# Kernel tuning notes

Hardware: AMD Instinct MI355X
Metric: run time of the kernel (lower is better)

The kernel has to match this reference:

```python
import jax, jax.numpy as jnp
import numpy as np

D_MODEL = 1024
HEADS = 16
D_K = D_MODEL // HEADS
D_FF = 4096
B, S = 2, 2048
EPS = 1e-5


def setup_inputs() -> dict:
    key = jax.random.key(0)
    ks = jax.random.split(key, 16)
    sc_att = 1.0 / np.sqrt(D_MODEL)
    sc_ff1 = 1.0 / np.sqrt(D_MODEL)
    sc_ff2 = 1.0 / np.sqrt(D_FF)
    return {
        "input": jax.random.normal(ks[0], (B, S, D_MODEL), jnp.float32),
        "mask": jnp.ones((B, 1, 1, S), jnp.int32),
        # stacked per-head projections: [H, D_MODEL, D_K]
        "Wq": jax.random.normal(ks[1], (HEADS, D_MODEL, D_K), jnp.float32) * sc_att,
        "bq": jax.random.normal(ks[2], (HEADS, D_K), jnp.float32) * 0.01,
        "Wk": jax.random.normal(ks[3], (HEADS, D_MODEL, D_K), jnp.float32) * sc_att,
        "bk": jax.random.normal(ks[4], (HEADS, D_K), jnp.float32) * 0.01,
        "Wv": jax.random.normal(ks[5], (HEADS, D_MODEL, D_K), jnp.float32) * sc_att,
        "bv": jax.random.normal(ks[6], (HEADS, D_K), jnp.float32) * 0.01,
        "Wo": jax.random.normal(ks[7], (D_MODEL, D_MODEL), jnp.float32) * sc_att,
        "bo": jax.random.normal(ks[8], (D_MODEL,), jnp.float32) * 0.01,
        "ln1_g": jnp.ones((D_MODEL,), jnp.float32),
        "ln1_b": jnp.zeros((D_MODEL,), jnp.float32),
        "ln2_g": jnp.ones((D_MODEL,), jnp.float32),
        "ln2_b": jnp.zeros((D_MODEL,), jnp.float32),
        "W1": jax.random.normal(ks[9], (D_MODEL, D_FF), jnp.float32) * sc_ff1,
        "b1": jax.random.normal(ks[10], (D_FF,), jnp.float32) * 0.01,
        "W2": jax.random.normal(ks[11], (D_FF, D_MODEL), jnp.float32) * sc_ff2,
        "b2": jax.random.normal(ks[12], (D_MODEL,), jnp.float32) * 0.01,
    }


def _layernorm(x, g, b):
    mu = jnp.mean(x, axis=-1, keepdims=True)
    var = jnp.mean(jnp.square(x - mu), axis=-1, keepdims=True)
    return (x - mu) * jax.lax.rsqrt(var + EPS) * g + b


def reference(input, mask, Wq, bq, Wk, bk, Wv, bv, Wo, bo,
              ln1_g, ln1_b, ln2_g, ln2_b, W1, b1, W2, b2):
    x = input
    # per-head projections, stacked: [B,H,S,D_K]
    q = jnp.einsum('bsd,hdk->bhsk', x, Wq) + bq[None, :, None, :]
    k = jnp.einsum('bsd,hdk->bhsk', x, Wk) + bk[None, :, None, :]
    v = jnp.einsum('bsd,hdk->bhsk', x, Wv) + bv[None, :, None, :]
    scores = jnp.einsum('bhqk,bhsk->bhqs', q, k) / np.sqrt(D_K)  # [B,H,S,S]
    scores = jnp.where(mask == 0, jnp.float32(-1e9), scores)
    attn = jax.nn.softmax(scores, axis=-1)
    ctx = jnp.einsum('bhqs,bhsk->bhqk', attn, v)  # [B,H,S,D_K]
    # concat heads along feature dim (head h occupies slice h*D_K:(h+1)*D_K)
    ctx = jnp.transpose(ctx, (0, 2, 1, 3)).reshape(B, S, D_MODEL)
    att_out = ctx @ Wo + bo
    h = _layernorm(x + att_out, ln1_g, ln1_b)
    ff = jax.nn.relu(h @ W1 + b1) @ W2 + b2
    return _layernorm(h + ff, ln2_g, ln2_b)
```

## Files before the change

kernel.cpp:

```cpp
#include <hip/hip_runtime.h>
#include <cstdint>
#include <cstddef>

typedef unsigned short u16;
typedef unsigned int   u32;
typedef unsigned short u16x4 __attribute__((ext_vector_type(4)));
typedef unsigned short u16x8 __attribute__((ext_vector_type(8)));
typedef unsigned int   u32x2 __attribute__((ext_vector_type(2)));
typedef __bf16 bf16x8 __attribute__((ext_vector_type(8)));
typedef float f32x4 __attribute__((ext_vector_type(4)));

#define MFMA16(a, b, c) __builtin_amdgcn_mfma_f32_16x16x32_bf16((a), (b), (c), 0, 0, 0)

__device__ __forceinline__ float bf2f(u16 h) {
  union { unsigned u; float f; } v; v.u = ((unsigned)h) << 16; return v.f;
}
__device__ __forceinline__ u16 f2bf(float f) {
  union { float f; unsigned u; } v; v.f = f;
  unsigned r = v.u + 0x7fffu + ((v.u >> 16) & 1u);
  return (u16)(r >> 16);
}
__device__ __forceinline__ void gll16(const u16* g, u16* l) {
  __builtin_amdgcn_global_load_lds(
      (const __attribute__((address_space(1))) void*)g,
      (__attribute__((address_space(3))) void*)l, 16, 0, 0);
}
__device__ __forceinline__ float fast_exp2(float x) {
#if __has_builtin(__builtin_amdgcn_exp2f)
  return __builtin_amdgcn_exp2f(x);
#else
  return exp2f(x);
#endif
}

__global__ __launch_bounds__(256) void transpose_qkv(
    const float* __restrict__ Wq, const float* __restrict__ Wk,
    const float* __restrict__ Wv, u16* __restrict__ outb) {
  __shared__ u16 tile[32][33];
  const int z = blockIdx.z;
  const int which = z >> 4, h = z & 15;
  const float* in = (which == 0 ? Wq : (which == 1 ? Wk : Wv)) + (size_t)h * 1024 * 64;
  u16* out = outb + ((size_t)which * 1024 + h * 64) * 1024;
  const int tx = threadIdx.x & 31, ty = threadIdx.x >> 5;
  const int r0 = blockIdx.y * 32, c0 = blockIdx.x * 32;
  #pragma unroll
  for (int i = 0; i < 32; i += 8)
    tile[ty + i][tx] = f2bf(in[(size_t)(r0 + ty + i) * 64 + c0 + tx]);
  __syncthreads();
  #pragma unroll
  for (int i = 0; i < 32; i += 8)
    out[(size_t)(c0 + ty + i) * 1024 + r0 + tx] = tile[tx][ty + i];
}

__global__ __launch_bounds__(256) void transpose_w(
    const float* __restrict__ Wo, const float* __restrict__ W1,
    const float* __restrict__ W2, u16* __restrict__ Wo_t,
    u16* __restrict__ W1_t, u16* __restrict__ W2_t) {
  __shared__ u16 tile[32][33];
  const int id = blockIdx.x;
  const float* in; u16* outp; int R, C, cx, ry;
  if (id < 1024)      { in = Wo; outp = Wo_t; R = 1024; C = 1024; cx = id & 31;  ry = id >> 5; }
  else if (id < 5120) { int t = id - 1024; in = W1; outp = W1_t; R = 1024; C = 4096; cx = t & 127; ry = t >> 7; }
  else                { int t = id - 5120; in = W2; outp = W2_t; R = 4096; C = 1024; cx = t & 31;  ry = t >> 5; }
  const int tx = threadIdx.x & 31, ty = threadIdx.x >> 5;
  const int r0 = ry * 32, c0 = cx * 32;
  #pragma unroll
  for (int i = 0; i < 32; i += 8)
    tile[ty + i][tx] = f2bf(in[(size_t)(r0 + ty + i) * C + c0 + tx]);
  __syncthreads();
  #pragma unroll
  for (int i = 0; i < 32; i += 8)
    outp[(size_t)(c0 + ty + i) * R + r0 + tx] = tile[tx][ty + i];
}

__global__ __launch_bounds__(256) void prep_small(
    const float* __restrict__ bq, const float* __restrict__ bk,
    const float* __restrict__ bv, const int* __restrict__ mask,
    float* __restrict__ biasq, float* __restrict__ madd2) {
  int i = blockIdx.x * 256 + threadIdx.x;
  if (i < 3072) {
    biasq[i] = (i < 1024) ? bq[i] : (i < 2048 ? bk[i - 1024] : bv[i - 2048]);
  } else if (i < 7168) {
    int j = i - 3072;
    madd2[j] = mask[j] ? -23.083120f : -1.442695e9f;
  }
}

__global__ __launch_bounds__(256) void cvt_x(
    const float* __restrict__ in, u16* __restrict__ out, int n) {
  int i = (blockIdx.x * 256 + threadIdx.x) * 4;
  if (i >= n) return;
  const float4 v = *(const float4*)&in[i];
  u16x4 o;
  o[0] = f2bf(v.x); o[1] = f2bf(v.y); o[2] = f2bf(v.z); o[3] = f2bf(v.w);
  *(u16x4*)&out[i] = o;
}

template <int MODE>
__global__ __launch_bounds__(256) void gemm_bt(
    const u16* __restrict__ A, const u16* __restrict__ Bt,
    const float* __restrict__ bias, u16* __restrict__ C,
    int M, int N, int K) {
  __shared__ __align__(16) u16 As[2][128 * 32];
  __shared__ __align__(16) u16 Bs[2][128 * 32];
  const int tid = threadIdx.x;
  const int lane = tid & 63;
  const int wave = tid >> 6;
  const int m0 = blockIdx.y * 128;
  const int n0 = blockIdx.x * 128;
  const int wr = (wave >> 1) * 64;
  const int wc = (wave & 1) * 64;
  const int lrow = lane & 15;
  const int quad = lane >> 4;

  const int srow = lane >> 2;
  const int scol = (lane & 3) * 8;
  const u16* gA1 = &A[(size_t)(m0 + wave * 16 + srow) * K + scol];
  const u16* gA2 = &A[(size_t)(m0 + 64 + wave * 16 + srow) * K + scol];
  const u16* gB1 = &Bt[(size_t)(n0 + wave * 16 + srow) * K + scol];
  const u16* gB2 = &Bt[(size_t)(n0 + 64 + wave * 16 + srow) * K + scol];
  const int so1 = (wave * 16) * 32;
  const int so2 = (wave * 16 + 64) * 32;

  f32x4 acc[4][4];
  #pragma unroll
  for (int i = 0; i < 4; ++i)
    #pragma unroll
    for (int j = 0; j < 4; ++j)
      acc[i][j] = (f32x4){0.f, 0.f, 0.f, 0.f};

  for (int k0 = 0; k0 < K; k0 += 64) {
    gll16(gA1 + k0, &As[0][so1]);
    gll16(gA2 + k0, &As[0][so2]);
    gll16(gB1 + k0, &Bs[0][so1]);
    gll16(gB2 + k0, &Bs[0][so2]);
    gll16(gA1 + k0 + 32, &As[1][so1]);
    gll16(gA2 + k0 + 32, &As[1][so2]);
    gll16(gB1 + k0 + 32, &Bs[1][so1]);
    gll16(gB2 + k0 + 32, &Bs[1][so2]);
    __syncthreads();
    #pragma unroll
    for (int kb = 0; kb < 2; ++kb) {
      bf16x8 af[4], bfr[4];
      #pragma unroll
      for (int i = 0; i < 4; ++i) {
        af[i]  = *(const bf16x8*)&As[kb][(wr + i * 16 + lrow) * 32 + quad * 8];
        bfr[i] = *(const bf16x8*)&Bs[kb][(wc + i * 16 + lrow) * 32 + quad * 8];
      }
      #pragma unroll
      for (int fr = 0; fr < 4; ++fr)
        #pragma unroll
        for (int fc = 0; fc < 4; ++fc)
          acc[fr][fc] = MFMA16(af[fr], bfr[fc], acc[fr][fc]);
    }
    __syncthreads();
  }

  #pragma unroll
  for (int fr = 0; fr < 4; ++fr) {
    int rowb = m0 + wr + fr * 16 + quad * 4;
    #pragma unroll
    for (int fc = 0; fc < 4; ++fc) {
      int col = n0 + wc + fc * 16 + lrow;
      float bv = bias[col];
      #pragma unroll
      for (int r = 0; r < 4; ++r) {
        float v = acc[fr][fc][r] + bv;
        if (MODE == 1) v = fmaxf(v, 0.f);
        C[(size_t)(rowb + r) * N + col] = f2bf(v);
      }
    }
  }
}

__global__ __launch_bounds__(256) void gemm_splitk(
    const u16* __restrict__ A, const u16* __restrict__ Bt,
    u16* __restrict__ Cp, int M, int N, int K) {
  __shared__ __align__(16) u16 As[2][128 * 32];
  __shared__ __align__(16) u16 Bs[2][128 * 32];
  const int tid = threadIdx.x;
  const int lane = tid & 63;
  const int wave = tid >> 6;
  const int m0 = blockIdx.y * 128;
  const int n0 = blockIdx.x * 128;
  const int kz = blockIdx.z;
  const int Kh = K >> 1;
  const int kbase = kz * Kh;
  const int wr = (wave >> 1) * 64;
  const int wc = (wave & 1) * 64;
  const int lrow = lane & 15;
  const int quad = lane >> 4;

  const int srow = lane >> 2;
  const int scol = (lane & 3) * 8;
  const u16* gA1 = &A[(size_t)(m0 + wave * 16 + srow) * K + kbase + scol];
  const u16* gA2 = &A[(size_t)(m0 + 64 + wave * 16 + srow) * K + kbase + scol];
  const u16* gB1 = &Bt[(size_t)(n0 + wave * 16 + srow) * K + kbase + scol];
  const u16* gB2 = &Bt[(size_t)(n0 + 64 + wave * 16 + srow) * K + kbase + scol];
  const int so1 = (wave * 16) * 32;
  const int so2 = (wave * 16 + 64) * 32;
  u16* C = Cp + (size_t)kz * M * N;

  f32x4 acc[4][4];
  #pragma unroll
  for (int i = 0; i < 4; ++i)
    #pragma unroll
    for (int j = 0; j < 4; ++j)
      acc[i][j] = (f32x4){0.f, 0.f, 0.f, 0.f};

  for (int k0 = 0; k0 < Kh; k0 += 64) {
    gll16(gA1 + k0, &As[0][so1]);
    gll16(gA2 + k0, &As[0][so2]);
    gll16(gB1 + k0, &Bs[0][so1]);
    gll16(gB2 + k0, &Bs[0][so2]);
    gll16(gA1 + k0 + 32, &As[1][so1]);
    gll16(gA2 + k0 + 32, &As[1][so2]);
    gll16(gB1 + k0 + 32, &Bs[1][so1]);
    gll16(gB2 + k0 + 32, &Bs[1][so2]);
    __syncthreads();
    #pragma unroll
    for (int kb = 0; kb < 2; ++kb) {
      bf16x8 af[4], bfr[4];
      #pragma unroll
      for (int i = 0; i < 4; ++i) {
        af[i]  = *(const bf16x8*)&As[kb][(wr + i * 16 + lrow) * 32 + quad * 8];
        bfr[i] = *(const bf16x8*)&Bs[kb][(wc + i * 16 + lrow) * 32 + quad * 8];
      }
      #pragma unroll
      for (int fr = 0; fr < 4; ++fr)
        #pragma unroll
        for (int fc = 0; fc < 4; ++fc)
          acc[fr][fc] = MFMA16(af[fr], bfr[fc], acc[fr][fc]);
    }
    __syncthreads();
  }

  #pragma unroll
  for (int fr = 0; fr < 4; ++fr) {
    int rowb = m0 + wr + fr * 16 + quad * 4;
    #pragma unroll
    for (int fc = 0; fc < 4; ++fc) {
      int col = n0 + wc + fc * 16 + lrow;
      #pragma unroll
      for (int r = 0; r < 4; ++r)
        C[(size_t)(rowb + r) * N + col] = f2bf(acc[fr][fc][r]);
    }
  }
}

__global__ __launch_bounds__(256) void attn_kernel(
    const u16* __restrict__ xqkv, const float* __restrict__ madd2,
    u16* __restrict__ ctx) {
  __shared__ __align__(16) u16 Ks[64][72];
  __shared__ __align__(16) u16 Vt[64][136];
  __shared__ __align__(16) u16 Ps[4][2][16][72];
  const int tid = threadIdx.x;
  const int lane = tid & 63;
  const int wave = tid >> 6;
  const int lrow = lane & 15;
  const int quad = lane >> 4;
  const int b = blockIdx.z, h = blockIdx.y;
  const int qb = blockIdx.x * 128 + wave * 16;
  const u16* Qp = xqkv + (size_t)b * 2048 * 3072 + h * 64;
  const u16* Kp = Qp + 1024;
  const u16* Vp = Qp + 2048;
  const float S2 = 0.18033688f;

  bf16x8 qa[2][2];
  #pragma unroll
  for (int t = 0; t < 2; ++t) {
    qa[t][0] = *(const bf16x8*)&Qp[(size_t)(qb + t * 64 + lrow) * 3072 + quad * 8];
    qa[t][1] = *(const bf16x8*)&Qp[(size_t)(qb + t * 64 + lrow) * 3072 + 32 + quad * 8];
  }

  f32x4 o[2][4];
  #pragma unroll
  for (int t = 0; t < 2; ++t)
    #pragma unroll
    for (int i = 0; i < 4; ++i) o[t][i] = (f32x4){0.f, 0.f, 0.f, 0.f};
  float rsum[2] = {0.f, 0.f};

  const int ks_row = tid >> 3, ks_col = (tid & 7) * 8;
  const int v_dg = tid >> 4;
  const int v_kp = tid & 15;
  const float* maddb = madd2 + b * 2048;

  u16x8 kreg[2];
  u16x4 va[2], vb[2];
  #pragma unroll
  for (int sh = 0; sh < 2; ++sh) {
    kreg[sh] = *(const u16x8*)&Kp[(size_t)(sh * 32 + ks_row) * 3072 + ks_col];
    va[sh] = *(const u16x4*)&Vp[(size_t)(sh * 32 + 2 * v_kp) * 3072 + v_dg * 4];
    vb[sh] = *(const u16x4*)&Vp[(size_t)(sh * 32 + 2 * v_kp + 1) * 3072 + v_dg * 4];
  }

  for (int s0 = 0; s0 < 2048; s0 += 64) {
    __syncthreads();
    #pragma unroll
    for (int sh = 0; sh < 2; ++sh) {
      *(u16x8*)&Ks[sh * 32 + ks_row][ks_col] = kreg[sh];
      #pragma unroll
      for (int j = 0; j < 4; ++j) {
        u32 pk = ((u32)vb[sh][j] << 16) | (u32)va[sh][j];
        *(u32*)&Vt[v_dg * 4 + j][sh * 32 + 2 * v_kp] = pk;
      }
    }
    __syncthreads();
    if (s0 + 64 < 2048) {
      #pragma unroll
      for (int sh = 0; sh < 2; ++sh) {
        int sb = s0 + 64 + sh * 32;
        kreg[sh] = *(const u16x8*)&Kp[(size_t)(sb + ks_row) * 3072 + ks_col];
        va[sh] = *(const u16x4*)&Vp[(size_t)(sb + 2 * v_kp) * 3072 + v_dg * 4];
        vb[sh] = *(const u16x4*)&Vp[(size_t)(sb + 2 * v_kp + 1) * 3072 + v_dg * 4];
      }
    }

    bf16x8 kf[4][2], vf[4][2];
    #pragma unroll
    for (int kb = 0; kb < 4; ++kb) {
      kf[kb][0] = *(const bf16x8*)&Ks[kb * 16 + lrow][quad * 8];
      kf[kb][1] = *(const bf16x8*)&Ks[kb * 16 + lrow][32 + quad * 8];
    }
    #pragma unroll
    for (int nb = 0; nb < 4; ++nb) {
      vf[nb][0] = *(const bf16x8*)&Vt[nb * 16 + lrow][quad * 8];
      vf[nb][1] = *(const bf16x8*)&Vt[nb * 16 + lrow][32 + quad * 8];
    }

    #pragma unroll
    for (int t = 0; t < 2; ++t) {
      #pragma unroll
      for (int kb = 0; kb < 4; ++kb) {
        f32x4 z = (f32x4){0.f, 0.f, 0.f, 0.f};
        z = MFMA16(kf[kb][0], qa[t][0], z);
        z = MFMA16(kf[kb][1], qa[t][1], z);
        f32x4 m4 = *(const f32x4*)&maddb[s0 + kb * 16 + quad * 4];
        u32 pb[4];
        #pragma unroll
        for (int r = 0; r < 4; ++r) {
          float p = fast_exp2(fmaf(z[r], S2, m4[r]));
          rsum[t] += p;
          union { float f; u32 u; } cv; cv.f = p;
          pb[r] = cv.u + 0x8000u;
        }
        u32x2 w2;
        w2[0] = __builtin_amdgcn_perm(pb[1], pb[0], 0x07060302);
        w2[1] = __builtin_amdgcn_perm(pb[3], pb[2], 0x07060302);
        *(u32x2*)&Ps[wave][t][lrow][kb * 16 + quad * 4] = w2;
      }
      #pragma unroll
      for (int kh = 0; kh < 2; ++kh) {
        bf16x8 pa = *(const bf16x8*)&Ps[wave][t][lrow][kh * 32 + quad * 8];
        #pragma unroll
        for (int nb = 0; nb < 4; ++nb)
          o[t][nb] = MFMA16(pa, vf[nb][kh], o[t][nb]);
      }
    }
  }

  #pragma unroll
  for (int t = 0; t < 2; ++t) {
    float rs = rsum[t];
    rs += __shfl_xor(rs, 16, 64);
    rs += __shfl_xor(rs, 32, 64);
    float inv = 1.f / fmaxf(rs, 1e-30f);
    #pragma unroll
    for (int r = 0; r < 4; ++r) {
      float invq = __shfl(inv, quad * 4 + r, 64);
      int q = qb + t * 64 + quad * 4 + r;
      #pragma unroll
      for (int nb = 0; nb < 4; ++nb) {
        float v = o[t][nb][r] * invq;
        ctx[((size_t)b * 2048 + q) * 1024 + h * 64 + nb * 16 + lrow] = f2bf(v);
      }
    }
  }
}

template <int IN_BF, int OUT_BF>
__global__ __launch_bounds__(256) void add_ln2p(
    const void* __restrict__ xa_, const u16* __restrict__ p0,
    const u16* __restrict__ p1, const float* __restrict__ cb,
    const float* __restrict__ g, const float* __restrict__ bb,
    void* __restrict__ outp_) {
  __shared__ float red[8];
  const int tid = threadIdx.x;
  const size_t base = (size_t)blockIdx.x * 1024;
  const float* xf = (const float*)xa_;
  const u16*   xb = (const u16*)xa_;
  float v[4];
  float s = 0.f;
  #pragma unroll
  for (int i = 0; i < 4; ++i) {
    int c = i * 256 + tid;
    float xv = IN_BF ? bf2f(xb[base + c]) : xf[base + c];
    v[i] = xv + bf2f(p0[base + c]) + bf2f(p1[base + c]) + cb[c];
    s += v[i];
  }
  #pragma unroll
  for (int off = 32; off > 0; off >>= 1) s += __shfl_down(s, off, 64);
  if ((tid & 63) == 0) red[tid >> 6] = s;
  __syncthreads();
  float mean = (red[0] + red[1] + red[2] + red[3]) * (1.f / 1024.f);
  float s2 = 0.f;
  #pragma unroll
  for (int i = 0; i < 4; ++i) { float d = v[i] - mean; s2 += d * d; }
  #pragma unroll
  for (int off = 32; off > 0; off >>= 1) s2 += __shfl_down(s2, off, 64);
  if ((tid & 63) == 0) red[4 + (tid >> 6)] = s2;
  __syncthreads();
  float var = (red[4] + red[5] + red[6] + red[7]) * (1.f / 1024.f);
  float rstd = rsqrtf(var + 1e-5f);
  #pragma unroll
  for (int i = 0; i < 4; ++i) {
    int c = i * 256 + tid;
    float r = (v[i] - mean) * rstd * g[c] + bb[c];
    if (OUT_BF) ((u16*)outp_)[base + c] = f2bf(r);
    else        ((float*)outp_)[base + c] = r;
  }
}

extern "C" void kernel_launch(void* const* d_in, const int* in_sizes, int n_in,
                              void* d_out, int out_size, void* d_ws, size_t ws_size,
                              hipStream_t stream) {
  (void)in_sizes; (void)n_in; (void)out_size; (void)ws_size;
  const float* x    = (const float*)d_in[0];
  const int*   mask = (const int*)d_in[1];
  const float* Wq   = (const float*)d_in[2];
  const float* bq   = (const float*)d_in[3];
  const float* Wk   = (const float*)d_in[4];
  const float* bk   = (const float*)d_in[5];
  const float* Wv   = (const float*)d_in[6];
  const float* bv   = (const float*)d_in[7];
  const float* Wo   = (const float*)d_in[8];
  const float* bo   = (const float*)d_in[9];
  const float* ln1g = (const float*)d_in[10];
  const float* ln1b = (const float*)d_in[11];
  const float* ln2g = (const float*)d_in[12];
  const float* ln2b = (const float*)d_in[13];
  const float* W1   = (const float*)d_in[14];
  const float* b1   = (const float*)d_in[15];
  const float* W2   = (const float*)d_in[16];
  const float* b2   = (const float*)d_in[17];
  float* out = (float*)d_out;

  char* ws = (char*)d_ws;
  u16*   Wqkv_t = (u16*)(ws + 0);
  u16*   fp     = (u16*)(ws + 0);
  u16*   Wo_t   = (u16*)(ws + 6291456);
  u16*   W1_t   = (u16*)(ws + 8388608);
  u16*   W2_t   = (u16*)(ws + 16777216);
  u16*   xqkv   = (u16*)(ws + 25165824);
  u16*   wp     = (u16*)(ws + 25165824);
  u16*   xb     = (u16*)(ws + 50331648);
  u16*   ctx    = (u16*)(ws + 50331648);
  u16*   ff1    = (u16*)(ws + 25165824);
  u16*   hbuf   = (u16*)(ws + 67108864);
  float* biasq  = (float*)(ws + 75497472);
  float* madd2  = (float*)(ws + 75509760);

  prep_small<<<28, 256, 0, stream>>>(bq, bk, bv, mask, biasq, madd2);
  transpose_qkv<<<dim3(2, 32, 48), 256, 0, stream>>>(Wq, Wk, Wv, Wqkv_t);
  transpose_w<<<9216, 256, 0, stream>>>(Wo, W1, W2, Wo_t, W1_t, W2_t);
  cvt_x<<<4096, 256, 0, stream>>>(x, xb, 4194304);

  gemm_bt<0><<<dim3(24, 32), 256, 0, stream>>>(xb, Wqkv_t, biasq, xqkv,
                                               4096, 3072, 1024);
  attn_kernel<<<dim3(16, 16, 2), 256, 0, stream>>>(xqkv, madd2, ctx);
  gemm_splitk<<<dim3(8, 32, 2), 256, 0, stream>>>(ctx, Wo_t, wp, 4096, 1024, 1024);
  add_ln2p<0, 1><<<4096, 256, 0, stream>>>(x, wp, wp + 4194304, bo,
                                           ln1g, ln1b, hbuf);
  gemm_bt<1><<<dim3(32, 32), 256, 0, stream>>>(hbuf, W1_t, b1, ff1,
                                               4096, 4096, 1024);
  gemm_splitk<<<dim3(8, 32, 2), 256, 0, stream>>>(ff1, W2_t, fp, 4096, 1024, 4096);
  add_ln2p<1, 0><<<4096, 256, 0, stream>>>(hbuf, fp, fp + 4194304, b2,
                                           ln2g, ln2b, out);
}
```

Before: 379.2 us.

## Fold softmax scale into Q weights, halve attention rows per block, add MFMA priority

```diff
diff --git a/kernel.cpp b/kernel.cpp
--- a/kernel.cpp
+++ b/kernel.cpp
@@ -41,11 +41,12 @@
   const int which = z >> 4, h = z & 15;
   const float* in = (which == 0 ? Wq : (which == 1 ? Wk : Wv)) + (size_t)h * 1024 * 64;
   u16* out = outb + ((size_t)which * 1024 + h * 64) * 1024;
+  const float sc = (which == 0) ? 0.18033688f : 1.0f;
   const int tx = threadIdx.x & 31, ty = threadIdx.x >> 5;
   const int r0 = blockIdx.y * 32, c0 = blockIdx.x * 32;
   #pragma unroll
   for (int i = 0; i < 32; i += 8)
-    tile[ty + i][tx] = f2bf(in[(size_t)(r0 + ty + i) * 64 + c0 + tx]);
+    tile[ty + i][tx] = f2bf(in[(size_t)(r0 + ty + i) * 64 + c0 + tx] * sc);
   __syncthreads();
   #pragma unroll
   for (int i = 0; i < 32; i += 8)
@@ -79,7 +80,8 @@
     float* __restrict__ biasq, float* __restrict__ madd2) {
   int i = blockIdx.x * 256 + threadIdx.x;
   if (i < 3072) {
-    biasq[i] = (i < 1024) ? bq[i] : (i < 2048 ? bk[i - 1024] : bv[i - 2048]);
+    biasq[i] = (i < 1024) ? bq[i] * 0.18033688f
+                          : (i < 2048 ? bk[i - 1024] : bv[i - 2048]);
   } else if (i < 7168) {
     int j = i - 3072;
     madd2[j] = mask[j] ? -23.083120f : -1.442695e9f;
@@ -253,32 +255,25 @@
     u16* __restrict__ ctx) {
   __shared__ __align__(16) u16 Ks[64][72];
   __shared__ __align__(16) u16 Vt[64][136];
-  __shared__ __align__(16) u16 Ps[4][2][16][72];
+  __shared__ __align__(16) u16 Ps[4][16][72];
   const int tid = threadIdx.x;
   const int lane = tid & 63;
   const int wave = tid >> 6;
   const int lrow = lane & 15;
   const int quad = lane >> 4;
   const int b = blockIdx.z, h = blockIdx.y;
-  const int qb = blockIdx.x * 128 + wave * 16;
+  const int qb = blockIdx.x * 64 + wave * 16;
   const u16* Qp = xqkv + (size_t)b * 2048 * 3072 + h * 64;
   const u16* Kp = Qp + 1024;
   const u16* Vp = Qp + 2048;
-  const float S2 = 0.18033688f;
-
-  bf16x8 qa[2][2];
-  #pragma unroll
-  for (int t = 0; t < 2; ++t) {
-    qa[t][0] = *(const bf16x8*)&Qp[(size_t)(qb + t * 64 + lrow) * 3072 + quad * 8];
-    qa[t][1] = *(const bf16x8*)&Qp[(size_t)(qb + t * 64 + lrow) * 3072 + 32 + quad * 8];
-  }
-
-  f32x4 o[2][4];
-  #pragma unroll
-  for (int t = 0; t < 2; ++t)
-    #pragma unroll
-    for (int i = 0; i < 4; ++i) o[t][i] = (f32x4){0.f, 0.f, 0.f, 0.f};
-  float rsum[2] = {0.f, 0.f};
+
+  bf16x8 qa0 = *(const bf16x8*)&Qp[(size_t)(qb + lrow) * 3072 + quad * 8];
+  bf16x8 qa1 = *(const bf16x8*)&Qp[(size_t)(qb + lrow) * 3072 + 32 + quad * 8];
+
+  f32x4 o[4];
+  #pragma unroll
+  for (int i = 0; i < 4; ++i) o[i] = (f32x4){0.f, 0.f, 0.f, 0.f};
+  float rsum = 0.f;
 
   const int ks_row = tid >> 3, ks_col = (tid & 7) * 8;
   const int v_dg = tid >> 4;
@@ -329,51 +324,49 @@
     }
 
     #pragma unroll
-    for (int t = 0; t < 2; ++t) {
-      #pragma unroll
-      for (int kb = 0; kb < 4; ++kb) {
-        f32x4 z = (f32x4){0.f, 0.f, 0.f, 0.f};
-        z = MFMA16(kf[kb][0], qa[t][0], z);
-        z = MFMA16(kf[kb][1], qa[t][1], z);
-        f32x4 m4 = *(const f32x4*)&maddb[s0 + kb * 16 + quad * 4];
-        u32 pb[4];
-        #pragma unroll
-        for (int r = 0; r < 4; ++r) {
-          float p = fast_exp2(fmaf(z[r], S2, m4[r]));
-          rsum[t] += p;
-          union { float f; u32 u; } cv; cv.f = p;
-          pb[r] = cv.u + 0x8000u;
-        }
-        u32x2 w2;
-        w2[0] = __builtin_amdgcn_perm(pb[1], pb[0], 0x07060302);
-        w2[1] = __builtin_amdgcn_perm(pb[3], pb[2], 0x07060302);
-        *(u32x2*)&Ps[wave][t][lrow][kb * 16 + quad * 4] = w2;
-      }
-      #pragma unroll
-      for (int kh = 0; kh < 2; ++kh) {
-        bf16x8 pa = *(const bf16x8*)&Ps[wave][t][lrow][kh * 32 + quad * 8];
-        #pragma unroll
-        for (int nb = 0; nb < 4; ++nb)
-          o[t][nb] = MFMA16(pa, vf[nb][kh], o[t][nb]);
-      }
-    }
-  }
-
-  #pragma unroll
-  for (int t = 0; t < 2; ++t) {
-    float rs = rsum[t];
-    rs += __shfl_xor(rs, 16, 64);
-    rs += __shfl_xor(rs, 32, 64);
-    float inv = 1.f / fmaxf(rs, 1e-30f);
-    #pragma unroll
-    for (int r = 0; r < 4; ++r) {
-      float invq = __shfl(inv, quad * 4 + r, 64);
-      int q = qb + t * 64 + quad * 4 + r;
-      #pragma unroll
-      for (int nb = 0; nb < 4; ++nb) {
-        float v = o[t][nb][r] * invq;
-        ctx[((size_t)b * 2048 + q) * 1024 + h * 64 + nb * 16 + lrow] = f2bf(v);
-      }
+    for (int kb = 0; kb < 4; ++kb) {
+      f32x4 z = (f32x4){0.f, 0.f, 0.f, 0.f};
+      __builtin_amdgcn_s_setprio(1);
+      z = MFMA16(kf[kb][0], qa0, z);
+      z = MFMA16(kf[kb][1], qa1, z);
+      __builtin_amdgcn_s_setprio(0);
+      f32x4 m4 = *(const f32x4*)&maddb[s0 + kb * 16 + quad * 4];
+      u32 pb[4];
+      #pragma unroll
+      for (int r = 0; r < 4; ++r) {
+        float p = fast_exp2(z[r] + m4[r]);
+        rsum += p;
+        union { float f; u32 u; } cv; cv.f = p;
+        pb[r] = cv.u + 0x8000u;
+      }
+      u32x2 w2;
+      w2[0] = __builtin_amdgcn_perm(pb[1], pb[0], 0x07060302);
+      w2[1] = __builtin_amdgcn_perm(pb[3], pb[2], 0x07060302);
+      *(u32x2*)&Ps[wave][lrow][kb * 16 + quad * 4] = w2;
+    }
+    #pragma unroll
+    for (int kh = 0; kh < 2; ++kh) {
+      bf16x8 pa = *(const bf16x8*)&Ps[wave][lrow][kh * 32 + quad * 8];
+      __builtin_amdgcn_s_setprio(1);
+      #pragma unroll
+      for (int nb = 0; nb < 4; ++nb)
+        o[nb] = MFMA16(pa, vf[nb][kh], o[nb]);
+      __builtin_amdgcn_s_setprio(0);
+    }
+  }
+
+  float rs = rsum;
+  rs += __shfl_xor(rs, 16, 64);
+  rs += __shfl_xor(rs, 32, 64);
+  float inv = 1.f / fmaxf(rs, 1e-30f);
+  #pragma unroll
+  for (int r = 0; r < 4; ++r) {
+    float invq = __shfl(inv, quad * 4 + r, 64);
+    int q = qb + quad * 4 + r;
+    #pragma unroll
+    for (int nb = 0; nb < 4; ++nb) {
+      float v = o[nb][r] * invq;
+      ctx[((size_t)b * 2048 + q) * 1024 + h * 64 + nb * 16 + lrow] = f2bf(v);
     }
   }
 }
@@ -467,7 +460,7 @@
 
   gemm_bt<0><<<dim3(24, 32), 256, 0, stream>>>(xb, Wqkv_t, biasq, xqkv,
                                                4096, 3072, 1024);
-  attn_kernel<<<dim3(16, 16, 2), 256, 0, stream>>>(xqkv, madd2, ctx);
+  attn_kernel<<<dim3(32, 16, 2), 256, 0, stream>>>(xqkv, madd2, ctx);
   gemm_splitk<<<dim3(8, 32, 2), 256, 0, stream>>>(ctx, Wo_t, wp, 4096, 1024, 1024);
   add_ln2p<0, 1><<<4096, 256, 0, stream>>>(x, wp, wp + 4194304, bo,
                                            ln1g, ln1b, hbuf);
```

New measurement: 451.8 us. +19.2%, slower.

## Split attention over two key halves with a separate combine kernel

Applied to the files above, without the earlier changes.

```diff
diff --git a/kernel.cpp b/kernel.cpp
--- a/kernel.cpp
+++ b/kernel.cpp
@@ -41,11 +41,12 @@
   const int which = z >> 4, h = z & 15;
   const float* in = (which == 0 ? Wq : (which == 1 ? Wk : Wv)) + (size_t)h * 1024 * 64;
   u16* out = outb + ((size_t)which * 1024 + h * 64) * 1024;
+  const float sc = (which == 0) ? 0.18033688f : 1.0f;
   const int tx = threadIdx.x & 31, ty = threadIdx.x >> 5;
   const int r0 = blockIdx.y * 32, c0 = blockIdx.x * 32;
   #pragma unroll
   for (int i = 0; i < 32; i += 8)
-    tile[ty + i][tx] = f2bf(in[(size_t)(r0 + ty + i) * 64 + c0 + tx]);
+    tile[ty + i][tx] = f2bf(in[(size_t)(r0 + ty + i) * 64 + c0 + tx] * sc);
   __syncthreads();
   #pragma unroll
   for (int i = 0; i < 32; i += 8)
@@ -79,7 +80,8 @@
     float* __restrict__ biasq, float* __restrict__ madd2) {
   int i = blockIdx.x * 256 + threadIdx.x;
   if (i < 3072) {
-    biasq[i] = (i < 1024) ? bq[i] : (i < 2048 ? bk[i - 1024] : bv[i - 2048]);
+    biasq[i] = (i < 1024) ? bq[i] * 0.18033688f
+                          : (i < 2048 ? bk[i - 1024] : bv[i - 2048]);
   } else if (i < 7168) {
     int j = i - 3072;
     madd2[j] = mask[j] ? -23.083120f : -1.442695e9f;
@@ -250,21 +252,25 @@
 
 __global__ __launch_bounds__(256) void attn_kernel(
     const u16* __restrict__ xqkv, const float* __restrict__ madd2,
-    u16* __restrict__ ctx) {
+    u16* __restrict__ op0, u16* __restrict__ op1,
+    float* __restrict__ rsums) {
   __shared__ __align__(16) u16 Ks[64][72];
-  __shared__ __align__(16) u16 Vt[64][136];
+  __shared__ __align__(16) u16 Vt[64][72];
   __shared__ __align__(16) u16 Ps[4][2][16][72];
   const int tid = threadIdx.x;
   const int lane = tid & 63;
   const int wave = tid >> 6;
   const int lrow = lane & 15;
   const int quad = lane >> 4;
-  const int b = blockIdx.z, h = blockIdx.y;
+  const int bz = blockIdx.z;
+  const int b = bz >> 1, ph = bz & 1;
+  const int h = blockIdx.y;
   const int qb = blockIdx.x * 128 + wave * 16;
+  const int kbase0 = ph * 1024;
   const u16* Qp = xqkv + (size_t)b * 2048 * 3072 + h * 64;
   const u16* Kp = Qp + 1024;
   const u16* Vp = Qp + 2048;
-  const float S2 = 0.18033688f;
+  u16* opP = ph ? op1 : op0;
 
   bf16x8 qa[2][2];
   #pragma unroll
@@ -289,12 +295,12 @@
   u16x4 va[2], vb[2];
   #pragma unroll
   for (int sh = 0; sh < 2; ++sh) {
-    kreg[sh] = *(const u16x8*)&Kp[(size_t)(sh * 32 + ks_row) * 3072 + ks_col];
-    va[sh] = *(const u16x4*)&Vp[(size_t)(sh * 32 + 2 * v_kp) * 3072 + v_dg * 4];
-    vb[sh] = *(const u16x4*)&Vp[(size_t)(sh * 32 + 2 * v_kp + 1) * 3072 + v_dg * 4];
-  }
-
-  for (int s0 = 0; s0 < 2048; s0 += 64) {
+    kreg[sh] = *(const u16x8*)&Kp[(size_t)(kbase0 + sh * 32 + ks_row) * 3072 + ks_col];
+    va[sh] = *(const u16x4*)&Vp[(size_t)(kbase0 + sh * 32 + 2 * v_kp) * 3072 + v_dg * 4];
+    vb[sh] = *(const u16x4*)&Vp[(size_t)(kbase0 + sh * 32 + 2 * v_kp + 1) * 3072 + v_dg * 4];
+  }
+
+  for (int s0 = kbase0; s0 < kbase0 + 1024; s0 += 64) {
     __syncthreads();
     #pragma unroll
     for (int sh = 0; sh < 2; ++sh) {
@@ -306,7 +312,7 @@
       }
     }
     __syncthreads();
-    if (s0 + 64 < 2048) {
+    if (s0 + 64 < kbase0 + 1024) {
       #pragma unroll
       for (int sh = 0; sh < 2; ++sh) {
         int sb = s0 + 64 + sh * 32;
@@ -333,13 +339,15 @@
       #pragma unroll
       for (int kb = 0; kb < 4; ++kb) {
         f32x4 z = (f32x4){0.f, 0.f, 0.f, 0.f};
+        __builtin_amdgcn_s_setprio(1);
         z = MFMA16(kf[kb][0], qa[t][0], z);
         z = MFMA16(kf[kb][1], qa[t][1], z);
+        __builtin_amdgcn_s_setprio(0);
         f32x4 m4 = *(const f32x4*)&maddb[s0 + kb * 16 + quad * 4];
         u32 pb[4];
         #pragma unroll
         for (int r = 0; r < 4; ++r) {
-          float p = fast_exp2(fmaf(z[r], S2, m4[r]));
+          float p = fast_exp2(z[r] + m4[r]);
           rsum[t] += p;
           union { float f; u32 u; } cv; cv.f = p;
           pb[r] = cv.u + 0x8000u;
@@ -352,9 +360,11 @@
       #pragma unroll
       for (int kh = 0; kh < 2; ++kh) {
         bf16x8 pa = *(const bf16x8*)&Ps[wave][t][lrow][kh * 32 + quad * 8];
+        __builtin_amdgcn_s_setprio(1);
         #pragma unroll
         for (int nb = 0; nb < 4; ++nb)
           o[t][nb] = MFMA16(pa, vf[nb][kh], o[t][nb]);
+        __builtin_amdgcn_s_setprio(0);
       }
     }
   }
@@ -364,18 +374,35 @@
     float rs = rsum[t];
     rs += __shfl_xor(rs, 16, 64);
     rs += __shfl_xor(rs, 32, 64);
-    float inv = 1.f / fmaxf(rs, 1e-30f);
+    if (quad == 0)
+      rsums[(((size_t)b * 2048 + qb + t * 64 + lrow) * 16 + h) * 2 + ph] = rs;
     #pragma unroll
     for (int r = 0; r < 4; ++r) {
-      float invq = __shfl(inv, quad * 4 + r, 64);
       int q = qb + t * 64 + quad * 4 + r;
       #pragma unroll
-      for (int nb = 0; nb < 4; ++nb) {
-        float v = o[t][nb][r] * invq;
-        ctx[((size_t)b * 2048 + q) * 1024 + h * 64 + nb * 16 + lrow] = f2bf(v);
-      }
-    }
-  }
+      for (int nb = 0; nb < 4; ++nb)
+        opP[((size_t)b * 2048 + q) * 1024 + h * 64 + nb * 16 + lrow] =
+            f2bf(o[t][nb][r]);
+    }
+  }
+}
+
+__global__ __launch_bounds__(256) void attn_combine(
+    const u16* __restrict__ op0, const u16* __restrict__ op1,
+    const float* __restrict__ rsums, u16* __restrict__ ctx) {
+  int i = (blockIdx.x * 256 + threadIdx.x) * 4;
+  int row = i >> 10;
+  int h = (i & 1023) >> 6;
+  float r0 = rsums[((size_t)row * 16 + h) * 2 + 0];
+  float r1 = rsums[((size_t)row * 16 + h) * 2 + 1];
+  float inv = 1.f / fmaxf(r0 + r1, 1e-30f);
+  u16x4 a = *(const u16x4*)&op0[i];
+  u16x4 c = *(const u16x4*)&op1[i];
+  u16x4 o;
+  #pragma unroll
+  for (int j = 0; j < 4; ++j)
+    o[j] = f2bf((bf2f(a[j]) + bf2f(c[j])) * inv);
+  *(u16x4*)&ctx[i] = o;
 }
 
 template <int IN_BF, int OUT_BF>
@@ -447,6 +474,7 @@
 
   char* ws = (char*)d_ws;
   u16*   Wqkv_t = (u16*)(ws + 0);
+  float* rsums  = (float*)(ws + 0);
   u16*   fp     = (u16*)(ws + 0);
   u16*   Wo_t   = (u16*)(ws + 6291456);
   u16*   W1_t   = (u16*)(ws + 8388608);
@@ -454,8 +482,10 @@
   u16*   xqkv   = (u16*)(ws + 25165824);
   u16*   wp     = (u16*)(ws + 25165824);
   u16*   xb     = (u16*)(ws + 50331648);
+  u16*   op0    = (u16*)(ws + 50331648);
   u16*   ctx    = (u16*)(ws + 50331648);
   u16*   ff1    = (u16*)(ws + 25165824);
+  u16*   op1    = (u16*)(ws + 67108864);
   u16*   hbuf   = (u16*)(ws + 67108864);
   float* biasq  = (float*)(ws + 75497472);
   float* madd2  = (float*)(ws + 75509760);
@@ -467,7 +497,8 @@
 
   gemm_bt<0><<<dim3(24, 32), 256, 0, stream>>>(xb, Wqkv_t, biasq, xqkv,
                                                4096, 3072, 1024);
-  attn_kernel<<<dim3(16, 16, 2), 256, 0, stream>>>(xqkv, madd2, ctx);
+  attn_kernel<<<dim3(16, 16, 4), 256, 0, stream>>>(xqkv, madd2, op0, op1, rsums);
+  attn_combine<<<4096, 256, 0, stream>>>(op0, op1, rsums, ctx);
   gemm_splitk<<<dim3(8, 32, 2), 256, 0, stream>>>(ctx, Wo_t, wp, 4096, 1024, 1024);
   add_ln2p<0, 1><<<4096, 256, 0, stream>>>(x, wp, wp + 4194304, bo,
                                            ln1g, ln1b, hbuf);
```

New measurement: 411.4 us. +8.5%, slower.

## Double-buffer K/V tiles in attention, fold softmax scale into Wq, add setprio

Applied to the files above, without the earlier changes.

```diff
diff --git a/kernel.cpp b/kernel.cpp
--- a/kernel.cpp
+++ b/kernel.cpp
@@ -41,11 +41,12 @@
   const int which = z >> 4, h = z & 15;
   const float* in = (which == 0 ? Wq : (which == 1 ? Wk : Wv)) + (size_t)h * 1024 * 64;
   u16* out = outb + ((size_t)which * 1024 + h * 64) * 1024;
+  const float sc = (which == 0) ? 0.18033688f : 1.0f;
   const int tx = threadIdx.x & 31, ty = threadIdx.x >> 5;
   const int r0 = blockIdx.y * 32, c0 = blockIdx.x * 32;
   #pragma unroll
   for (int i = 0; i < 32; i += 8)
-    tile[ty + i][tx] = f2bf(in[(size_t)(r0 + ty + i) * 64 + c0 + tx]);
+    tile[ty + i][tx] = f2bf(in[(size_t)(r0 + ty + i) * 64 + c0 + tx] * sc);
   __syncthreads();
   #pragma unroll
   for (int i = 0; i < 32; i += 8)
@@ -79,7 +80,8 @@
     float* __restrict__ biasq, float* __restrict__ madd2) {
   int i = blockIdx.x * 256 + threadIdx.x;
   if (i < 3072) {
-    biasq[i] = (i < 1024) ? bq[i] : (i < 2048 ? bk[i - 1024] : bv[i - 2048]);
+    biasq[i] = (i < 1024) ? bq[i] * 0.18033688f
+                          : (i < 2048 ? bk[i - 1024] : bv[i - 2048]);
   } else if (i < 7168) {
     int j = i - 3072;
     madd2[j] = mask[j] ? -23.083120f : -1.442695e9f;
@@ -251,8 +253,8 @@
 __global__ __launch_bounds__(256) void attn_kernel(
     const u16* __restrict__ xqkv, const float* __restrict__ madd2,
     u16* __restrict__ ctx) {
-  __shared__ __align__(16) u16 Ks[64][72];
-  __shared__ __align__(16) u16 Vt[64][136];
+  __shared__ __align__(16) u16 Ks[2][64][72];
+  __shared__ __align__(16) u16 Vt[2][64][72];
   __shared__ __align__(16) u16 Ps[4][2][16][72];
   const int tid = threadIdx.x;
   const int lane = tid & 63;
@@ -264,7 +266,6 @@
   const u16* Qp = xqkv + (size_t)b * 2048 * 3072 + h * 64;
   const u16* Kp = Qp + 1024;
   const u16* Vp = Qp + 2048;
-  const float S2 = 0.18033688f;
 
   bf16x8 qa[2][2];
   #pragma unroll
@@ -287,59 +288,75 @@
 
   u16x8 kreg[2];
   u16x4 va[2], vb[2];
+
   #pragma unroll
   for (int sh = 0; sh < 2; ++sh) {
     kreg[sh] = *(const u16x8*)&Kp[(size_t)(sh * 32 + ks_row) * 3072 + ks_col];
     va[sh] = *(const u16x4*)&Vp[(size_t)(sh * 32 + 2 * v_kp) * 3072 + v_dg * 4];
     vb[sh] = *(const u16x4*)&Vp[(size_t)(sh * 32 + 2 * v_kp + 1) * 3072 + v_dg * 4];
   }
+  #pragma unroll
+  for (int sh = 0; sh < 2; ++sh) {
+    *(u16x8*)&Ks[0][sh * 32 + ks_row][ks_col] = kreg[sh];
+    #pragma unroll
+    for (int j = 0; j < 4; ++j) {
+      u32 pk = ((u32)vb[sh][j] << 16) | (u32)va[sh][j];
+      *(u32*)&Vt[0][v_dg * 4 + j][sh * 32 + 2 * v_kp] = pk;
+    }
+  }
+  #pragma unroll
+  for (int sh = 0; sh < 2; ++sh) {
+    kreg[sh] = *(const u16x8*)&Kp[(size_t)(64 + sh * 32 + ks_row) * 3072 + ks_col];
+    va[sh] = *(const u16x4*)&Vp[(size_t)(64 + sh * 32 + 2 * v_kp) * 3072 + v_dg * 4];
+    vb[sh] = *(const u16x4*)&Vp[(size_t)(64 + sh * 32 + 2 * v_kp + 1) * 3072 + v_dg * 4];
+  }
+  __syncthreads();
 
   for (int s0 = 0; s0 < 2048; s0 += 64) {
-    __syncthreads();
-    #pragma unroll
-    for (int sh = 0; sh < 2; ++sh) {
-      *(u16x8*)&Ks[sh * 32 + ks_row][ks_col] = kreg[sh];
-      #pragma unroll
-      for (int j = 0; j < 4; ++j) {
-        u32 pk = ((u32)vb[sh][j] << 16) | (u32)va[sh][j];
-        *(u32*)&Vt[v_dg * 4 + j][sh * 32 + 2 * v_kp] = pk;
-      }
-    }
-    __syncthreads();
+    const int cur = (s0 >> 6) & 1;
+    bf16x8 kf[4][2], vf[4][2];
+    #pragma unroll
+    for (int kb = 0; kb < 4; ++kb) {
+      kf[kb][0] = *(const bf16x8*)&Ks[cur][kb * 16 + lrow][quad * 8];
+      kf[kb][1] = *(const bf16x8*)&Ks[cur][kb * 16 + lrow][32 + quad * 8];
+      vf[kb][0] = *(const bf16x8*)&Vt[cur][kb * 16 + lrow][quad * 8];
+      vf[kb][1] = *(const bf16x8*)&Vt[cur][kb * 16 + lrow][32 + quad * 8];
+    }
     if (s0 + 64 < 2048) {
       #pragma unroll
       for (int sh = 0; sh < 2; ++sh) {
-        int sb = s0 + 64 + sh * 32;
+        *(u16x8*)&Ks[cur ^ 1][sh * 32 + ks_row][ks_col] = kreg[sh];
+        #pragma unroll
+        for (int j = 0; j < 4; ++j) {
+          u32 pk = ((u32)vb[sh][j] << 16) | (u32)va[sh][j];
+          *(u32*)&Vt[cur ^ 1][v_dg * 4 + j][sh * 32 + 2 * v_kp] = pk;
+        }
+      }
+    }
+    if (s0 + 128 < 2048) {
+      #pragma unroll
+      for (int sh = 0; sh < 2; ++sh) {
+        int sb = s0 + 128 + sh * 32;
         kreg[sh] = *(const u16x8*)&Kp[(size_t)(sb + ks_row) * 3072 + ks_col];
         va[sh] = *(const u16x4*)&Vp[(size_t)(sb + 2 * v_kp) * 3072 + v_dg * 4];
         vb[sh] = *(const u16x4*)&Vp[(size_t)(sb + 2 * v_kp + 1) * 3072 + v_dg * 4];
       }
     }
 
-    bf16x8 kf[4][2], vf[4][2];
-    #pragma unroll
-    for (int kb = 0; kb < 4; ++kb) {
-      kf[kb][0] = *(const bf16x8*)&Ks[kb * 16 + lrow][quad * 8];
-      kf[kb][1] = *(const bf16x8*)&Ks[kb * 16 + lrow][32 + quad * 8];
-    }
-    #pragma unroll
-    for (int nb = 0; nb < 4; ++nb) {
-      vf[nb][0] = *(const bf16x8*)&Vt[nb * 16 + lrow][quad * 8];
-      vf[nb][1] = *(const bf16x8*)&Vt[nb * 16 + lrow][32 + quad * 8];
-    }
-
     #pragma unroll
     for (int t = 0; t < 2; ++t) {
       #pragma unroll
       for (int kb = 0; kb < 4; ++kb) {
         f32x4 z = (f32x4){0.f, 0.f, 0.f, 0.f};
+        __builtin_amdgcn_s_setprio(1);
         z = MFMA16(kf[kb][0], qa[t][0], z);
         z = MFMA16(kf[kb][1], qa[t][1], z);
+        __builtin_amdgcn_s_setprio(0);
         f32x4 m4 = *(const f32x4*)&maddb[s0 + kb * 16 + quad * 4];
         u32 pb[4];
         #pragma unroll
         for (int r = 0; r < 4; ++r) {
-          float p = fast_exp2(fmaf(z[r], S2, m4[r]));
+          float p = fast_exp2(z[r] + m4[r]);
           rsum[t] += p;
           union { float f; u32 u; } cv; cv.f = p;
           pb[r] = cv.u + 0x8000u;
@@ -352,11 +369,14 @@
       #pragma unroll
       for (int kh = 0; kh < 2; ++kh) {
         bf16x8 pa = *(const bf16x8*)&Ps[wave][t][lrow][kh * 32 + quad * 8];
+        __builtin_amdgcn_s_setprio(1);
         #pragma unroll
         for (int nb = 0; nb < 4; ++nb)
           o[t][nb] = MFMA16(pa, vf[nb][kh], o[t][nb]);
-      }
-    }
+        __builtin_amdgcn_s_setprio(0);
+      }
+    }
+    __syncthreads();
   }
 
   #pragma unroll
```

Measured after the change: 407.1 us. 1.07x slower.
